# Performance work log

Measured on AMD Instinct MI355X. Metric: run time of the kernel, lower is better.

The kernel has to match this reference:

```python
import jax, jax.numpy as jnp
import numpy as np

BETA = 8.0  # inverse temperature from __init__


def setup_inputs() -> dict:
    key = jax.random.key(0)
    k1, k2 = jax.random.split(key)
    B, N, D = 2048, 100000, 512
    query = jax.random.normal(k1, (B, D), dtype=jnp.float32)
    memory = jax.random.normal(k2, (N, D), dtype=jnp.float32)
    return {"query": query, "memory": memory, "steps": 2}


def reference(query, memory, steps):
    # Iterative modern-Hopfield retrieval (normalize=False path):
    # x <- sigmoid(softmax(beta * x @ M^T) @ M), repeated `steps` times.
    x = query.astype(jnp.float32)
    for _ in range(int(steps)):
        logits = BETA * jnp.einsum('bd,nd->bn', x, memory)   # [B, N]
        attn = jax.nn.softmax(logits, axis=-1)               # [B, N]
        x = jax.nn.sigmoid(jnp.einsum('bn,nd->bd', attn, memory))  # [B, D]
    return x
```

## Files before the change

### kernel.cpp

```cpp
#include <hip/hip_runtime.h>


#define B_ROWS 2048
#define DDIM   512
#define NTOT   100000
#define NPAD   100096
#define QB256  8
#define NT256  391
#define PT256  32
#define CAP    2048
#define SCAP   512
#define MARGIN 35.0f
#define WCUT   15.0f

typedef int   i32x4 __attribute__((ext_vector_type(4)));

#define VMCNT(n) asm volatile("s_waitcnt vmcnt(" #n ")" ::: "memory")
#define LGK0()   asm volatile("s_waitcnt lgkmcnt(0)" ::: "memory")
#define BARR()   do { __builtin_amdgcn_s_barrier(); asm volatile("" ::: "memory"); } while(0)

__device__ inline unsigned encf(float f){
  unsigned u = __float_as_uint(f);
  return (u & 0x80000000u) ? ~u : (u | 0x80000000u);
}
__device__ inline float decf(unsigned u){
  unsigned v = (u & 0x80000000u) ? (u ^ 0x80000000u) : ~u;
  return __uint_as_float(v);
}
__device__ inline void llds16(const void* g, void* l){
  __builtin_amdgcn_global_load_lds(
      (const __attribute__((address_space(1))) unsigned int*)(unsigned long long)g,
      (__attribute__((address_space(3))) unsigned int*)(unsigned long long)l,
      16, 0, 0);
}
__device__ inline unsigned q4(float a, float b, float c, float d, float mult){
  int qa = (int)fmaxf(-127.f, fminf(127.f, rintf(a*mult)));
  int qb = (int)fmaxf(-127.f, fminf(127.f, rintf(b*mult)));
  int qc = (int)fmaxf(-127.f, fminf(127.f, rintf(c*mult)));
  int qd = (int)fmaxf(-127.f, fminf(127.f, rintf(d*mult)));
  return (qa & 0xff) | ((qb & 0xff) << 8) | ((qc & 0xff) << 16) | ((qd & 0xff) << 24);
}

__global__ void cvt_i8(const float* __restrict__ src, signed char* __restrict__ dst,
                       long nsrc, long ndst, float mult){
  long i = ((long)blockIdx.x * blockDim.x + threadIdx.x) * 16;
  if (i >= ndst) return;
  uint4 o;
  if (i < nsrc){
    const float4* p = (const float4*)(src + i);
    float4 a = p[0], b = p[1], c = p[2], d = p[3];
    o.x = q4(a.x, a.y, a.z, a.w, mult);
    o.y = q4(b.x, b.y, b.z, b.w, mult);
    o.z = q4(c.x, c.y, c.z, c.w, mult);
    o.w = q4(d.x, d.y, d.z, d.w, mult);
  } else { o.x = o.y = o.z = o.w = 0u; }
  *(uint4*)(dst + i) = o;
}

__global__ void init_stats(unsigned* __restrict__ m0u, unsigned* __restrict__ cnt){
  int i = blockIdx.x * blockDim.x + threadIdx.x;
  if (i < B_ROWS){ m0u[i] = 0u; cnt[i] = 0u; }
}

template<int MODE>
__launch_bounds__(512, 2)
__global__ void gemm_tile(const signed char* __restrict__ A,
                          const signed char* __restrict__ Bm,
                          unsigned* __restrict__ m0u,
                          unsigned* __restrict__ cnt,
                          int* __restrict__ cand,
                          float dq){
  extern __shared__ signed char smem[];
  __shared__ float tt[256];

  const int qblk = blockIdx.x, nblk = blockIdx.y;
  const int tid  = threadIdx.x;
  const int lane = tid & 63, wave = tid >> 6;
  const int wr = wave >> 2, wc = wave & 3;
  const int quad = lane >> 4, l15 = lane & 15;

  if (MODE == 1 && tid < 256) tt[tid] = decf(m0u[qblk*256 + tid]) - MARGIN;

  const int srow = wave*16 + (lane >> 2);
  const int sc   = (lane & 3) ^ ((lane >> 3) & 3);
  const signed char* gA0 = A  + (size_t)(qblk*256 + srow)*DDIM + sc*16;
  const signed char* gA1 = gA0 + (size_t)128*DDIM;
  const signed char* gB0 = Bm + (size_t)(nblk*256 + srow)*DDIM + sc*16;
  const signed char* gB1 = gB0 + (size_t)128*DDIM;

  const int swz = (quad ^ ((l15 >> 1) & 3)) << 4;
  int offA[8], offB[4];
  #pragma unroll
  for (int i = 0; i < 8; i++) offA[i] = (wr*128 + i*16 + l15)*64 + swz;
  #pragma unroll
  for (int j = 0; j < 4; j++) offB[j] = 16384 + (wc*64 + j*16 + l15)*64 + swz;

  i32x4 acc[8][4] = {};

  auto STAGE = [&](int kb, int b){
    signed char* lb = smem + b*32768;
    const size_t o = (size_t)kb*64;
    llds16(gA0 + o, lb + wave*1024);
    llds16(gA1 + o, lb + 8192  + wave*1024);
    llds16(gB0 + o, lb + 16384 + wave*1024);
    llds16(gB1 + o, lb + 16384 + 8192 + wave*1024);
  };

  STAGE(0, 0); STAGE(1, 1);
  VMCNT(4); BARR();

  #pragma unroll
  for (int t = 0; t < 8; ++t){
    const int cb = t % 3;
    if (t + 2 < 8) STAGE(t + 2, (t + 2) % 3);
    const signed char* bb = smem + cb*32768;
    i32x4 bf[4], af[8];
    #pragma unroll
    for (int j = 0; j < 4; j++) bf[j] = *(const i32x4*)(bb + offB[j]);
    #pragma unroll
    for (int i = 0; i < 8; i++) af[i] = *(const i32x4*)(bb + offA[i]);
    __builtin_amdgcn_s_setprio(1);
    #pragma unroll
    for (int i = 0; i < 8; i++)
      #pragma unroll
      for (int j = 0; j < 4; j++)
        acc[i][j] = __builtin_amdgcn_mfma_i32_16x16x64_i8(af[i], bf[j], acc[i][j], 0, 0, 0);
    __builtin_amdgcn_s_setprio(0);
    if (t < 7){
      LGK0();
      if (t < 6) { VMCNT(4); } else { VMCNT(0); }
      BARR();
    }
  }

  if (MODE == 0){
    #pragma unroll
    for (int i = 0; i < 8; i++){
      #pragma unroll
      for (int r = 0; r < 4; r++){
        float v = fmaxf(fmaxf((float)acc[i][0][r], (float)acc[i][1][r]),
                        fmaxf((float)acc[i][2][r], (float)acc[i][3][r])) * dq;
        #pragma unroll
        for (int m = 1; m < 16; m <<= 1) v = fmaxf(v, __shfl_xor(v, m));
        if (l15 == 0){
          int row = qblk*256 + wr*128 + i*16 + quad*4 + r;
          atomicMax(&m0u[row], encf(v));
        }
      }
    }
  } else {
    const int nbase = nblk*256 + wc*64 + l15;
    #pragma unroll
    for (int i = 0; i < 8; i++){
      #pragma unroll
      for (int r = 0; r < 4; r++){
        const int lrow = wr*128 + i*16 + quad*4 + r;
        const float th = tt[lrow];
        #pragma unroll
        for (int j = 0; j < 4; j++){
          float v = (float)acc[i][j][r] * dq;
          int n = nbase + j*16;
          if (v > th && n < NTOT){
            int q = qblk*256 + lrow;
            unsigned pos = atomicAdd(&cnt[q], 1u);
            if (pos < CAP) cand[(size_t)q*CAP + pos] = n;
          }
        }
      }
    }
  }
}

__global__ void finalize_row(const float* __restrict__ xin, const float* __restrict__ M,
                             const int* __restrict__ cand, const unsigned* __restrict__ cnt,
                             float* __restrict__ xout){
  __shared__ float xs[DDIM];
  __shared__ float lc[CAP];
  __shared__ int   sv[SCAP];
  __shared__ float mred[4];
  __shared__ int   ns;
  const int q = blockIdx.x, tid = threadIdx.x;
  const int wave = tid >> 6, lane = tid & 63;
  xs[tid]       = xin[(size_t)q*DDIM + tid];
  xs[tid + 256] = xin[(size_t)q*DDIM + 256 + tid];
  if (tid == 0) ns = 0;
  const unsigned cq = cnt[q];
  const int c0 = (int)(cq < (unsigned)CAP ? cq : (unsigned)CAP);
  __syncthreads();

  for (int c = wave; c < c0; c += 4){
    const float* Mr = M + (size_t)cand[(size_t)q*CAP + c]*DDIM;
    float s = 0.f;
    #pragma unroll
    for (int k = 0; k < 8; k++) s += xs[lane + 64*k] * Mr[lane + 64*k];
    #pragma unroll
    for (int o = 32; o; o >>= 1) s += __shfl_xor(s, o);
    if (lane == 0) lc[c] = 8.0f * s;
  }
  __syncthreads();

  float m = -3.0e38f;
  for (int c = tid; c < c0; c += 256) m = fmaxf(m, lc[c]);
  #pragma unroll
  for (int o = 32; o; o >>= 1) m = fmaxf(m, __shfl_xor(m, o));
  if (lane == 0) mred[wave] = m;
  __syncthreads();
  m = fmaxf(fmaxf(mred[0], mred[1]), fmaxf(mred[2], mred[3]));

  for (int c = tid; c < c0; c += 256){
    if (lc[c] > m - WCUT){
      int p = atomicAdd(&ns, 1);
      if (p < SCAP) sv[p] = c;
    }
  }
  __syncthreads();
  const int nsv = ns < SCAP ? ns : SCAP;

  float Z = 0.f, a0 = 0.f, a1 = 0.f;
  for (int i = 0; i < nsv; i++){
    const int c = sv[i];
    const float w = expf(lc[c] - m);
    const float* Mr = M + (size_t)cand[(size_t)q*CAP + c]*DDIM;
    Z  += w;
    a0 += w * Mr[tid];
    a1 += w * Mr[tid + 256];
  }
  xout[(size_t)q*DDIM + tid]       = 1.f/(1.f + expf(-a0/Z));
  xout[(size_t)q*DDIM + tid + 256] = 1.f/(1.f + expf(-a1/Z));
}

extern "C" void kernel_launch(void* const* d_in, const int* in_sizes, int n_in,
                              void* d_out, int out_size, void* d_ws, size_t ws_size,
                              hipStream_t stream){
  const float* query = (const float*)d_in[0];
  const float* M     = (const float*)d_in[1];
  float* out = (float*)d_out;

  char* w = (char*)d_ws;
  size_t off = 0;
  signed char* Bq   = (signed char*)(w + off); off += (size_t)NPAD*DDIM;
  signed char* Aq   = (signed char*)(w + off); off += (size_t)B_ROWS*DDIM;
  float*       xbuf = (float*)(w + off);       off += (size_t)B_ROWS*DDIM*4;
  unsigned*    m0u  = (unsigned*)(w + off);    off += (size_t)B_ROWS*4;
  unsigned*    cnt  = (unsigned*)(w + off);    off += (size_t)B_ROWS*4;
  int*         cand = (int*)(w + off);         off += (size_t)B_ROWS*CAP*4;
  if (ws_size < off) return;

  hipFuncSetAttribute((const void*)gemm_tile<0>,
                      hipFuncAttributeMaxDynamicSharedMemorySize, 3*32768);
  hipFuncSetAttribute((const void*)gemm_tile<1>,
                      hipFuncAttributeMaxDynamicSharedMemorySize, 3*32768);

  const float MCLIP = 4.0f;
  cvt_i8<<<(long)NPAD*DDIM/16/256, 256, 0, stream>>>(M, Bq, (long)NTOT*DDIM, (long)NPAD*DDIM,
                                                     127.0f/MCLIP);

  for (int step = 0; step < 2; ++step){
    const float* x = step ? (const float*)xbuf : query;
    float*       y = step ? out : xbuf;
    const float ACLIP = step ? 8.0f : 40.0f;
    const float multA = 8.0f * 127.0f / ACLIP;
    const float dq    = (ACLIP/127.0f) * (MCLIP/127.0f);
    init_stats<<<8, 256, 0, stream>>>(m0u, cnt);
    cvt_i8<<<(long)B_ROWS*DDIM/16/256, 256, 0, stream>>>(x, Aq, (long)B_ROWS*DDIM,
                                                         (long)B_ROWS*DDIM, multA);
    gemm_tile<0><<<dim3(QB256, PT256), 512, 3*32768, stream>>>(Aq, Bq, m0u, cnt, cand, dq);
    gemm_tile<1><<<dim3(QB256, NT256), 512, 3*32768, stream>>>(Aq, Bq, m0u, cnt, cand, dq);
    finalize_row<<<B_ROWS, 256, 0, stream>>>(x, M, cand, cnt, y);
  }
}
```

Baseline: 756.0 us.

## Interleave GEMM MFMA quadrants with staged loads, use 4-buffer LDS ring, XCD-aware block remap

The int8 GEMM main loop now issues its MFMAs as four quadrant phases. Each phase loads only the LDS fragments it needs and issues one global-to-LDS prefetch unit for stage t+2, so memory traffic spreads across the compute. The LDS ring grows from 3 to 4 buffers, which makes the reuse distance safe under the finer barriers. The launch grid is flattened to 1D with a block-id remap so consecutive blocks on one XCD share query or memory tiles for better L2 locality. The extra barriers and sched_barriers add synchronisation overhead, and the larger LDS footprint could limit occupancy.

```diff
diff --git a/kernel.cpp b/kernel.cpp
--- a/kernel.cpp
+++ b/kernel.cpp
@@ -17,6 +17,7 @@
 
 #define VMCNT(n) asm volatile("s_waitcnt vmcnt(" #n ")" ::: "memory")
 #define LGK0()   asm volatile("s_waitcnt lgkmcnt(0)" ::: "memory")
+#define SCHED0() __builtin_amdgcn_sched_barrier(0)
 #define BARR()   do { __builtin_amdgcn_s_barrier(); asm volatile("" ::: "memory"); } while(0)
 
 __device__ inline unsigned encf(float f){
@@ -69,17 +70,19 @@
                           unsigned* __restrict__ m0u,
                           unsigned* __restrict__ cnt,
                           int* __restrict__ cand,
-                          float dq){
+                          float dq,
+                          int nbt){
   extern __shared__ signed char smem[];
   __shared__ float tt[256];
 
-  const int qblk = blockIdx.x, nblk = blockIdx.y;
+  const int bid = blockIdx.x;
+  const int w    = (bid & 7) * nbt + (bid >> 3);
+  const int qblk = w & 7, nblk = w >> 3;
+
   const int tid  = threadIdx.x;
   const int lane = tid & 63, wave = tid >> 6;
   const int wr = wave >> 2, wc = wave & 3;
   const int quad = lane >> 4, l15 = lane & 15;
-
-  if (MODE == 1 && tid < 256) tt[tid] = decf(m0u[qblk*256 + tid]) - MARGIN;
 
   const int srow = wave*16 + (lane >> 2);
   const int sc   = (lane & 3) ^ ((lane >> 3) & 3);
@@ -96,41 +99,78 @@
   for (int j = 0; j < 4; j++) offB[j] = 16384 + (wc*64 + j*16 + l15)*64 + swz;
 
   i32x4 acc[8][4] = {};
-
-  auto STAGE = [&](int kb, int b){
-    signed char* lb = smem + b*32768;
-    const size_t o = (size_t)kb*64;
-    llds16(gA0 + o, lb + wave*1024);
-    llds16(gA1 + o, lb + 8192  + wave*1024);
-    llds16(gB0 + o, lb + 16384 + wave*1024);
-    llds16(gB1 + o, lb + 16384 + 8192 + wave*1024);
+  i32x4 afA[4], afB[4], bfA[2], bfB[2];
+
+  auto SUNIT = [&](int t, int u){
+    signed char* lb = smem + (t & 3) * 32768;
+    const size_t o = (size_t)t * 64;
+    if (u == 0) llds16(gA0 + o, lb +         wave*1024);
+    if (u == 1) llds16(gA1 + o, lb +  8192 + wave*1024);
+    if (u == 2) llds16(gB0 + o, lb + 16384 + wave*1024);
+    if (u == 3) llds16(gB1 + o, lb + 24576 + wave*1024);
   };
 
-  STAGE(0, 0); STAGE(1, 1);
+  #pragma unroll
+  for (int u = 0; u < 4; ++u) SUNIT(0, u);
+  #pragma unroll
+  for (int u = 0; u < 4; ++u) SUNIT(1, u);
+  if (MODE == 1 && tid < 256) tt[tid] = decf(m0u[qblk*256 + tid]) - MARGIN;
   VMCNT(4); BARR();
 
   #pragma unroll
   for (int t = 0; t < 8; ++t){
-    const int cb = t % 3;
-    if (t + 2 < 8) STAGE(t + 2, (t + 2) % 3);
-    const signed char* bb = smem + cb*32768;
-    i32x4 bf[4], af[8];
-    #pragma unroll
-    for (int j = 0; j < 4; j++) bf[j] = *(const i32x4*)(bb + offB[j]);
-    #pragma unroll
-    for (int i = 0; i < 8; i++) af[i] = *(const i32x4*)(bb + offA[i]);
+    const signed char* bb = smem + (t & 3) * 32768;
+    #pragma unroll
+    for (int i = 0; i < 4; i++) afA[i] = *(const i32x4*)(bb + offA[i]);
+    bfA[0] = *(const i32x4*)(bb + offB[0]);
+    bfA[1] = *(const i32x4*)(bb + offB[1]);
+    if (t + 2 < 8) SUNIT(t + 2, 0);
+    BARR(); LGK0(); SCHED0();
     __builtin_amdgcn_s_setprio(1);
     #pragma unroll
-    for (int i = 0; i < 8; i++)
-      #pragma unroll
-      for (int j = 0; j < 4; j++)
-        acc[i][j] = __builtin_amdgcn_mfma_i32_16x16x64_i8(af[i], bf[j], acc[i][j], 0, 0, 0);
+    for (int i = 0; i < 4; i++)
+      #pragma unroll
+      for (int j = 0; j < 2; j++)
+        acc[i][j] = __builtin_amdgcn_mfma_i32_16x16x64_i8(afA[i], bfA[j], acc[i][j], 0, 0, 0);
+    __builtin_amdgcn_s_setprio(0);
+    BARR();
+    bfB[0] = *(const i32x4*)(bb + offB[2]);
+    bfB[1] = *(const i32x4*)(bb + offB[3]);
+    if (t + 2 < 8) SUNIT(t + 2, 1);
+    BARR(); LGK0(); SCHED0();
+    __builtin_amdgcn_s_setprio(1);
+    #pragma unroll
+    for (int i = 0; i < 4; i++)
+      #pragma unroll
+      for (int j = 0; j < 2; j++)
+        acc[i][2+j] = __builtin_amdgcn_mfma_i32_16x16x64_i8(afA[i], bfB[j], acc[i][2+j], 0, 0, 0);
+    __builtin_amdgcn_s_setprio(0);
+    BARR();
+    #pragma unroll
+    for (int i = 0; i < 4; i++) afB[i] = *(const i32x4*)(bb + offA[4+i]);
+    if (t + 2 < 8) SUNIT(t + 2, 2);
+    BARR(); LGK0(); SCHED0();
+    __builtin_amdgcn_s_setprio(1);
+    #pragma unroll
+    for (int i = 0; i < 4; i++)
+      #pragma unroll
+      for (int j = 0; j < 2; j++)
+        acc[4+i][j] = __builtin_amdgcn_mfma_i32_16x16x64_i8(afB[i], bfA[j], acc[4+i][j], 0, 0, 0);
+    __builtin_amdgcn_s_setprio(0);
+    BARR();
+    if (t + 2 < 8) SUNIT(t + 2, 3);
+    BARR(); LGK0(); SCHED0();
+    __builtin_amdgcn_s_setprio(1);
+    #pragma unroll
+    for (int i = 0; i < 4; i++)
+      #pragma unroll
+      for (int j = 0; j < 2; j++)
+        acc[4+i][2+j] = __builtin_amdgcn_mfma_i32_16x16x64_i8(afB[i], bfB[j], acc[4+i][2+j], 0, 0, 0);
     __builtin_amdgcn_s_setprio(0);
     if (t < 7){
-      LGK0();
       if (t < 6) { VMCNT(4); } else { VMCNT(0); }
-      BARR();
     }
+    BARR();
   }
 
   if (MODE == 0){
@@ -247,9 +287,9 @@
   if (ws_size < off) return;
 
   hipFuncSetAttribute((const void*)gemm_tile<0>,
-                      hipFuncAttributeMaxDynamicSharedMemorySize, 3*32768);
+                      hipFuncAttributeMaxDynamicSharedMemorySize, 4*32768);
   hipFuncSetAttribute((const void*)gemm_tile<1>,
-                      hipFuncAttributeMaxDynamicSharedMemorySize, 3*32768);
+                      hipFuncAttributeMaxDynamicSharedMemorySize, 4*32768);
 
   const float MCLIP = 4.0f;
   cvt_i8<<<(long)NPAD*DDIM/16/256, 256, 0, stream>>>(M, Bq, (long)NTOT*DDIM, (long)NPAD*DDIM,
@@ -264,8 +304,8 @@
     init_stats<<<8, 256, 0, stream>>>(m0u, cnt);
     cvt_i8<<<(long)B_ROWS*DDIM/16/256, 256, 0, stream>>>(x, Aq, (long)B_ROWS*DDIM,
                                                          (long)B_ROWS*DDIM, multA);
-    gemm_tile<0><<<dim3(QB256, PT256), 512, 3*32768, stream>>>(Aq, Bq, m0u, cnt, cand, dq);
-    gemm_tile<1><<<dim3(QB256, NT256), 512, 3*32768, stream>>>(Aq, Bq, m0u, cnt, cand, dq);
+    gemm_tile<0><<<8*PT256, 512, 4*32768, stream>>>(Aq, Bq, m0u, cnt, cand, dq, PT256);
+    gemm_tile<1><<<8*NT256, 512, 4*32768, stream>>>(Aq, Bq, m0u, cnt, cand, dq, NT256);
     finalize_row<<<B_ROWS, 256, 0, stream>>>(x, M, cand, cnt, y);
   }
 }
```

Measured after the change: 728.5 us. 1.04x faster.

## Shrink int8 GEMM tiles to 128x128 with XCD-aware 1D block mapping

Applied to the files above, without the earlier changes.

Reduces the int8 MFMA tile from 256x256 with 8 waves to 128x128 with 4 waves, and cuts LDS per stage in half. This allows more resident blocks and gives a finer-grained grid. Block IDs are remapped so that consecutive blocks on the same XCD cover contiguous (qblk, nblk) tiles, which should improve L2 locality. It also drops the explicit lgkmcnt wait before the barrier. In exchange, the smaller tiles reuse less data per byte loaded and issue more global loads. Removing the LDS wait may depend on compiler-inserted waits for correctness.

```diff
diff --git a/kernel.cpp b/kernel.cpp
--- a/kernel.cpp
+++ b/kernel.cpp
@@ -5,9 +5,9 @@
 #define DDIM   512
 #define NTOT   100000
 #define NPAD   100096
-#define QB256  8
-#define NT256  391
-#define PT256  32
+#define QB128  16
+#define NT128  782
+#define PT128  32
 #define CAP    2048
 #define SCAP   512
 #define MARGIN 35.0f
@@ -16,7 +16,6 @@
 typedef int   i32x4 __attribute__((ext_vector_type(4)));
 
 #define VMCNT(n) asm volatile("s_waitcnt vmcnt(" #n ")" ::: "memory")
-#define LGK0()   asm volatile("s_waitcnt lgkmcnt(0)" ::: "memory")
 #define BARR()   do { __builtin_amdgcn_s_barrier(); asm volatile("" ::: "memory"); } while(0)
 
 __device__ inline unsigned encf(float f){
@@ -63,71 +62,73 @@
 }
 
 template<int MODE>
-__launch_bounds__(512, 2)
+__launch_bounds__(256, 3)
 __global__ void gemm_tile(const signed char* __restrict__ A,
                           const signed char* __restrict__ Bm,
                           unsigned* __restrict__ m0u,
                           unsigned* __restrict__ cnt,
                           int* __restrict__ cand,
-                          float dq){
+                          float dq,
+                          int cpx){
   extern __shared__ signed char smem[];
-  __shared__ float tt[256];
-
-  const int qblk = blockIdx.x, nblk = blockIdx.y;
+  __shared__ float tt[128];
+
+  const int bid = blockIdx.x;
+  const int w    = (bid & 7) * cpx + (bid >> 3);
+  const int qblk = w & 15, nblk = w >> 4;
+
   const int tid  = threadIdx.x;
   const int lane = tid & 63, wave = tid >> 6;
-  const int wr = wave >> 2, wc = wave & 3;
+  const int wr = wave >> 1, wc = wave & 1;
   const int quad = lane >> 4, l15 = lane & 15;
 
-  if (MODE == 1 && tid < 256) tt[tid] = decf(m0u[qblk*256 + tid]) - MARGIN;
+  if (MODE == 1 && tid < 128) tt[tid] = decf(m0u[qblk*128 + tid]) - MARGIN;
 
   const int srow = wave*16 + (lane >> 2);
   const int sc   = (lane & 3) ^ ((lane >> 3) & 3);
-  const signed char* gA0 = A  + (size_t)(qblk*256 + srow)*DDIM + sc*16;
-  const signed char* gA1 = gA0 + (size_t)128*DDIM;
-  const signed char* gB0 = Bm + (size_t)(nblk*256 + srow)*DDIM + sc*16;
-  const signed char* gB1 = gB0 + (size_t)128*DDIM;
+  const signed char* gA0 = A  + (size_t)(qblk*128 + srow)*DDIM + sc*16;
+  const signed char* gA1 = gA0 + (size_t)64*DDIM;
+  const signed char* gB0 = Bm + (size_t)(nblk*128 + srow)*DDIM + sc*16;
+  const signed char* gB1 = gB0 + (size_t)64*DDIM;
 
   const int swz = (quad ^ ((l15 >> 1) & 3)) << 4;
-  int offA[8], offB[4];
-  #pragma unroll
-  for (int i = 0; i < 8; i++) offA[i] = (wr*128 + i*16 + l15)*64 + swz;
-  #pragma unroll
-  for (int j = 0; j < 4; j++) offB[j] = 16384 + (wc*64 + j*16 + l15)*64 + swz;
-
-  i32x4 acc[8][4] = {};
-
-  auto STAGE = [&](int kb, int b){
-    signed char* lb = smem + b*32768;
-    const size_t o = (size_t)kb*64;
-    llds16(gA0 + o, lb + wave*1024);
-    llds16(gA1 + o, lb + 8192  + wave*1024);
-    llds16(gB0 + o, lb + 16384 + wave*1024);
-    llds16(gB1 + o, lb + 16384 + 8192 + wave*1024);
+  int offA[4], offB[4];
+  #pragma unroll
+  for (int i = 0; i < 4; i++) offA[i] = (wr*64 + i*16 + l15)*64 + swz;
+  #pragma unroll
+  for (int j = 0; j < 4; j++) offB[j] = 8192 + (wc*64 + j*16 + l15)*64 + swz;
+
+  i32x4 acc[4][4] = {};
+
+  auto STAGE = [&](int t){
+    signed char* lb = smem + (t % 3) * 16384;
+    const size_t o = (size_t)t * 64;
+    llds16(gA0 + o, lb +         wave*1024);
+    llds16(gA1 + o, lb +  4096 + wave*1024);
+    llds16(gB0 + o, lb +  8192 + wave*1024);
+    llds16(gB1 + o, lb + 12288 + wave*1024);
   };
 
-  STAGE(0, 0); STAGE(1, 1);
+  STAGE(0); STAGE(1);
   VMCNT(4); BARR();
 
   #pragma unroll
   for (int t = 0; t < 8; ++t){
-    const int cb = t % 3;
-    if (t + 2 < 8) STAGE(t + 2, (t + 2) % 3);
-    const signed char* bb = smem + cb*32768;
-    i32x4 bf[4], af[8];
+    const signed char* bb = smem + (t % 3) * 16384;
+    if (t + 2 < 8) STAGE(t + 2);
+    i32x4 af[4], bf[4];
     #pragma unroll
     for (int j = 0; j < 4; j++) bf[j] = *(const i32x4*)(bb + offB[j]);
     #pragma unroll
-    for (int i = 0; i < 8; i++) af[i] = *(const i32x4*)(bb + offA[i]);
+    for (int i = 0; i < 4; i++) af[i] = *(const i32x4*)(bb + offA[i]);
     __builtin_amdgcn_s_setprio(1);
     #pragma unroll
-    for (int i = 0; i < 8; i++)
+    for (int i = 0; i < 4; i++)
       #pragma unroll
       for (int j = 0; j < 4; j++)
         acc[i][j] = __builtin_amdgcn_mfma_i32_16x16x64_i8(af[i], bf[j], acc[i][j], 0, 0, 0);
     __builtin_amdgcn_s_setprio(0);
     if (t < 7){
-      LGK0();
       if (t < 6) { VMCNT(4); } else { VMCNT(0); }
       BARR();
     }
@@ -135,7 +136,7 @@
 
   if (MODE == 0){
     #pragma unroll
-    for (int i = 0; i < 8; i++){
+    for (int i = 0; i < 4; i++){
       #pragma unroll
       for (int r = 0; r < 4; r++){
         float v = fmaxf(fmaxf((float)acc[i][0][r], (float)acc[i][1][r]),
@@ -143,25 +144,25 @@
         #pragma unroll
         for (int m = 1; m < 16; m <<= 1) v = fmaxf(v, __shfl_xor(v, m));
         if (l15 == 0){
-          int row = qblk*256 + wr*128 + i*16 + quad*4 + r;
+          int row = qblk*128 + wr*64 + i*16 + quad*4 + r;
           atomicMax(&m0u[row], encf(v));
         }
       }
     }
   } else {
-    const int nbase = nblk*256 + wc*64 + l15;
-    #pragma unroll
-    for (int i = 0; i < 8; i++){
+    const int nbase = nblk*128 + wc*64 + l15;
+    #pragma unroll
+    for (int i = 0; i < 4; i++){
       #pragma unroll
       for (int r = 0; r < 4; r++){
-        const int lrow = wr*128 + i*16 + quad*4 + r;
+        const int lrow = wr*64 + i*16 + quad*4 + r;
         const float th = tt[lrow];
         #pragma unroll
         for (int j = 0; j < 4; j++){
           float v = (float)acc[i][j][r] * dq;
           int n = nbase + j*16;
           if (v > th && n < NTOT){
-            int q = qblk*256 + lrow;
+            int q = qblk*128 + lrow;
             unsigned pos = atomicAdd(&cnt[q], 1u);
             if (pos < CAP) cand[(size_t)q*CAP + pos] = n;
           }
@@ -247,9 +248,9 @@
   if (ws_size < off) return;
 
   hipFuncSetAttribute((const void*)gemm_tile<0>,
-                      hipFuncAttributeMaxDynamicSharedMemorySize, 3*32768);
+                      hipFuncAttributeMaxDynamicSharedMemorySize, 3*16384);
   hipFuncSetAttribute((const void*)gemm_tile<1>,
-                      hipFuncAttributeMaxDynamicSharedMemorySize, 3*32768);
+                      hipFuncAttributeMaxDynamicSharedMemorySize, 3*16384);
 
   const float MCLIP = 4.0f;
   cvt_i8<<<(long)NPAD*DDIM/16/256, 256, 0, stream>>>(M, Bq, (long)NTOT*DDIM, (long)NPAD*DDIM,
@@ -264,8 +265,8 @@
     init_stats<<<8, 256, 0, stream>>>(m0u, cnt);
     cvt_i8<<<(long)B_ROWS*DDIM/16/256, 256, 0, stream>>>(x, Aq, (long)B_ROWS*DDIM,
                                                          (long)B_ROWS*DDIM, multA);
-    gemm_tile<0><<<dim3(QB256, PT256), 512, 3*32768, stream>>>(Aq, Bq, m0u, cnt, cand, dq);
-    gemm_tile<1><<<dim3(QB256, NT256), 512, 3*32768, stream>>>(Aq, Bq, m0u, cnt, cand, dq);
+    gemm_tile<0><<<16*PT128, 256, 3*16384, stream>>>(Aq, Bq, m0u, cnt, cand, dq, 16*PT128/8);
+    gemm_tile<1><<<16*NT128, 256, 3*16384, stream>>>(Aq, Bq, m0u, cnt, cand, dq, 16*NT128/8);
     finalize_row<<<B_ROWS, 256, 0, stream>>>(x, M, cand, cnt, y);
   }
 }
```

After: 653.6 us. 1.16x faster.
